# Optimization experiments

Measured on AMD Instinct MI355X. Metric: run time of the kernel, lower is better.

The kernel has to match this reference:

```python
import jax, jax.numpy as jnp
import numpy as np

# Grid / problem sizes (match init_kwargs)
B, D, H, W = 2, 64, 256, 256      # batch + spatial_shape
N = 524288                         # active voxels
IN_DIM, HID = 32, 32               # input_dim, hidden_dim
C_IN = IN_DIM + HID                # conv in-channels (64)
C_OUT = 4 * HID                    # conv out-channels (128)
OFFSETS = [(dz, dy, dx) for dz in (-1, 0, 1) for dy in (-1, 0, 1) for dx in (-1, 0, 1)]


def setup_inputs() -> dict:
    key = jax.random.key(0)
    ks = jax.random.split(key, 5)
    # Unique active-voxel coordinates: odd multiplier is a bijection mod 2^k grid size.
    total = B * D * H * W
    MULT = 2654435761  # odd => injective on arange(N) mod total (total is a power of 2)
    lin = (np.arange(N, dtype=np.int64) * MULT) % total
    b = lin // (D * H * W)
    r = lin % (D * H * W)
    z = r // (H * W)
    r = r % (H * W)
    y = r // W
    x = r % W
    coors = jnp.asarray(np.stack([b, z, y, x], axis=1).astype(np.int32))  # [N,4]
    x_features = jax.random.normal(ks[0], (N, IN_DIM), jnp.float32)
    h_features = jax.random.normal(ks[1], (N, HID), jnp.float32)
    c_features = jax.random.normal(ks[2], (N, HID), jnp.float32)
    weight = jax.random.normal(ks[3], (27, C_IN, C_OUT), jnp.float32) * 0.05
    bias = jax.random.normal(ks[4], (C_OUT,), jnp.float32) * 0.05
    return {"x_features": x_features, "h_features": h_features,
            "c_features": c_features, "weight": weight, "bias": bias,
            "coors": coors, "batch_size": B}


def _subm_conv3d(feats, weight, bias, coors):
    """Submanifold sparse 3x3x3 conv: output only at active sites;
    gather-GEMM-scatter via a dense coordinate->point-id map (the rulebook)."""
    b, z, y, x = coors[:, 0], coors[:, 1], coors[:, 2], coors[:, 3]
    pid = jnp.arange(N, dtype=jnp.int32)
    idx_map = jnp.full((B, D, H, W), -1, jnp.int32).at[b, z, y, x].set(pid)
    out = jnp.zeros((N, C_OUT), feats.dtype) + bias  # [N, 4*HID]
    for k, (dz, dy, dx) in enumerate(OFFSETS):
        nz, ny, nx = z + dz, y + dy, x + dx
        inb = (nz >= 0) & (nz < D) & (ny >= 0) & (ny < H) & (nx >= 0) & (nx < W)
        nid = idx_map[b, jnp.clip(nz, 0, D - 1), jnp.clip(ny, 0, H - 1), jnp.clip(nx, 0, W - 1)]
        nid = jnp.where(inb, nid, -1)
        valid = nid >= 0
        gathered = jnp.where(valid[:, None], feats[jnp.maximum(nid, 0)], 0.0)  # [N, C_IN]
        out = out + gathered @ weight[k]
    return out


def reference(x_features, h_features, c_features, weight, bias, coors, batch_size):
    combined = jnp.concatenate([x_features, h_features], axis=1)  # [N, C_IN]
    cc = _subm_conv3d(combined, weight, bias, coors)              # [N, 4*HID]
    cc_i, cc_f, cc_o, cc_g = jnp.split(cc, 4, axis=1)
    i = jax.nn.sigmoid(cc_i)
    f = jax.nn.sigmoid(cc_f)
    o = jax.nn.sigmoid(cc_o)
    g = jnp.tanh(cc_g)
    c_next = f * c_features + i * g
    h_next = o * jnp.tanh(c_next)
    return (h_next, c_next)
```

## Files before the change

### kernel.cpp

```cpp
#include <hip/hip_runtime.h>
#include <stdint.h>

#define N_PTS 524288
#define DQ 64
#define HQ 256
#define WQ 256
#define MAP_BYTES (2*DQ*HQ*WQ*4)
#define FEAT_BLOCKS ((N_PTS*8)/256)
#define WT_BLOCKS   ((27*64*128 + 255)/256)

typedef short bf8  __attribute__((ext_vector_type(8)));
typedef float f16v __attribute__((ext_vector_type(16)));

static __device__ __forceinline__ short f2bf(float f) {
    union { float f; uint32_t u; } v; v.f = f;
    return (short)((v.u + 0x7fffu + ((v.u >> 16) & 1u)) >> 16);
}
static __device__ __forceinline__ float fast_sigmoid(float x) {
    return 1.f / (1.f + __expf(-x));
}
static __device__ __forceinline__ float fast_tanh(float x) {
    return 1.f - 2.f / (__expf(2.f * x) + 1.f);
}

__global__ void k_prep(const float* __restrict__ xf, const float* __restrict__ hf,
                       const int* __restrict__ coors, const float* __restrict__ w,
                       short* __restrict__ fb, int* __restrict__ map,
                       short* __restrict__ wt, short* __restrict__ zp) {
    int b = blockIdx.x;
    if (b < FEAT_BLOCKS) {
        int t = b * 256 + threadIdx.x;
        int n = t >> 3, seg = t & 7;
        const float* src = (seg < 4) ? (xf + n*32 + seg*8) : (hf + n*32 + seg*8 - 32);
        float4 a = ((const float4*)src)[0];
        float4 bb = ((const float4*)src)[1];
        bf8 rv;
        rv[0]=f2bf(a.x); rv[1]=f2bf(a.y); rv[2]=f2bf(a.z); rv[3]=f2bf(a.w);
        rv[4]=f2bf(bb.x); rv[5]=f2bf(bb.y); rv[6]=f2bf(bb.z); rv[7]=f2bf(bb.w);
        ((bf8*)fb)[t] = rv;
        if (seg == 0) {
            int4 c = ((const int4*)coors)[n];
            map[((c.x*DQ + c.y)*HQ + c.z)*WQ + c.w] = n;
        }
    } else {
        int t = (b - FEAT_BLOCKS) * 256 + threadIdx.x;
        if (t < 27*64*128) {
            int jj = t & 7, c = (t >> 3) & 127, jg = (t >> 10) & 7, k = t >> 13;
            int j = jg*8 + jj;
            wt[t] = f2bf(w[(k*64 + j)*128 + c]);
        }
        if (b == FEAT_BLOCKS + WT_BLOCKS - 1 && threadIdx.x < 32)
            ((int4*)zp)[threadIdx.x] = int4{0,0,0,0};
    }
}

__launch_bounds__(256, 2)
__global__ void k_main(const int* __restrict__ map, const short* __restrict__ fb,
                       const short* __restrict__ wt, const float* __restrict__ bias,
                       const float* __restrict__ cfeat, const int* __restrict__ coors,
                       const short* __restrict__ zp, float* __restrict__ out)
{
    __shared__ short Wlds[2][8192];

    const int tid  = threadIdx.x;
    const int lane = tid & 63;
    const int wv   = tid >> 6;
    const int l31  = lane & 31;
    const int lhi  = lane >> 5;

    const int pbase = blockIdx.x * 256;
    const int p     = pbase + wv*64 + lane;

    const int4 cr = ((const int4*)coors)[p];
    const int mb0 = cr.x*DQ;

    auto probe = [&](int ko) -> int {
        int dz = ko/9 - 1, dy = (ko/3)%3 - 1, dxo = ko%3 - 1;
        int nz = cr.y + dz, ny = cr.z + dy, nx = cr.w + dxo;
        bool inb = ((unsigned)nz < (unsigned)DQ) & ((unsigned)ny < (unsigned)HQ) &
                   ((unsigned)nx < (unsigned)WQ);
        int cz = min(max(nz, 0), DQ-1);
        int cy = min(max(ny, 0), HQ-1);
        int cx = min(max(nx, 0), WQ-1);
        int nid = map[((mb0 + cz)*HQ + cy)*WQ + cx];
        return inb ? nid : -1;
    };

    auto stageW = [&](int ko) {
        const short* src = wt + ko*8192;
        #pragma unroll
        for (int i = 0; i < 4; i++) {
            int cb = i*256 + wv*64;
            __builtin_amdgcn_global_load_lds(
                (const __attribute__((address_space(1))) void*)(src + (size_t)(cb + lane)*8),
                (__attribute__((address_space(3))) void*)&Wlds[ko & 1][cb*8],
                16, 0, 0);
        }
    };

    auto gather = [&](int n0, int n1, bf8* dst) {
        const short* s0 = (n0 >= 0) ? (fb + (size_t)n0*64 + lhi*8) : (zp + lhi*8);
        const short* s1 = (n1 >= 0) ? (fb + (size_t)n1*64 + lhi*8) : (zp + lhi*8);
        #pragma unroll
        for (int j = 0; j < 4; j++) {
            dst[j]     = *(const bf8*)(s0 + j*16);
            dst[4 + j] = *(const bf8*)(s1 + j*16);
        }
    };

    f16v acc[2][4];
    #pragma unroll
    for (int mt = 0; mt < 2; mt++)
        #pragma unroll
        for (int ct = 0; ct < 4; ct++) {
            float bv = bias[ct*32 + l31];
            #pragma unroll
            for (int r = 0; r < 16; r++) acc[mt][ct][r] = bv;
        }

    stageW(0);
    int pA = probe(0);
    int pB = probe(1);
    int pr_old = probe(2);

    bf8 fA[8], fB[8];
    {
        int g0 = __shfl(pA, l31, 64);
        int g1 = __shfl(pA, l31 + 32, 64);
        gather(g0, g1, fA);
    }
    int g0n = __shfl(pB, l31, 64);
    int g1n = __shfl(pB, l31 + 32, 64);

    __builtin_amdgcn_sched_barrier(0);
    asm volatile("s_waitcnt vmcnt(0)" ::: "memory");
    __builtin_amdgcn_s_barrier();
    __builtin_amdgcn_sched_barrier(0);

#define ITER_BODY(KO, FA, FB)                                                     \
    {                                                                             \
        const int _ko = (KO);                                                     \
        if (_ko < 26) {                                                           \
            stageW(_ko + 1);                        \
            __builtin_amdgcn_sched_barrier(0);                                    \
            gather(g0n, g1n, FB);                 \
            __builtin_amdgcn_sched_barrier(0);                                    \
        }                                                                         \
        int pr_new = (_ko < 24) ? probe(_ko + 3) : -1;                \
        const int buf = _ko & 1;                                                  \
        _Pragma("unroll")                                                         \
        for (int ks = 0; ks < 4; ks++) {                                          \
            int jg = ks*2 + lhi;                                                  \
            const short* wb = &Wlds[buf][(jg*128 + l31)*8];                       \
            _Pragma("unroll")                                                     \
            for (int ct = 0; ct < 4; ct++) {                                      \
                bf8 b = *(const bf8*)(wb + ct*32*8);                              \
                acc[0][ct] = __builtin_amdgcn_mfma_f32_32x32x16_bf16(FA[ks],     b, acc[0][ct], 0, 0, 0); \
                acc[1][ct] = __builtin_amdgcn_mfma_f32_32x32x16_bf16(FA[4 + ks], b, acc[1][ct], 0, 0, 0); \
            }                                                                     \
        }                                                                         \
        if (_ko < 25) {                                 \
            g0n = __shfl(pr_old, l31, 64);                                        \
            g1n = __shfl(pr_old, l31 + 32, 64);                                   \
            pr_old = pr_new;                                                      \
        }                                                                         \
        if (_ko < 26) {                                                           \
            __builtin_amdgcn_sched_barrier(0);                                    \
            \
            if (_ko < 24) { asm volatile("s_waitcnt vmcnt(9)" ::: "memory"); }    \
            else          { asm volatile("s_waitcnt vmcnt(8)" ::: "memory"); }    \
            __builtin_amdgcn_s_barrier();                                         \
            __builtin_amdgcn_sched_barrier(0);                                    \
        }                                                                         \
    }

    #pragma unroll 1
    for (int ko = 0; ko < 26; ko += 2) {
        ITER_BODY(ko,     fA, fB)
        ITER_BODY(ko + 1, fB, fA)
    }
    ITER_BODY(26, fA, fB)
#undef ITER_BODY

    #pragma unroll
    for (int mt = 0; mt < 2; mt++) {
        #pragma unroll
        for (int r = 0; r < 16; r++) {
            int row = (r & 3) + 8*(r >> 2) + 4*lhi;
            int pp  = pbase + wv*64 + mt*32 + row;
            float gi = acc[mt][0][r];
            float gf = acc[mt][1][r];
            float go = acc[mt][2][r];
            float gg = acc[mt][3][r];
            float cv = cfeat[pp*32 + l31];
            float si = fast_sigmoid(gi);
            float sf = fast_sigmoid(gf);
            float so = fast_sigmoid(go);
            float tg = fast_tanh(gg);
            float cn = sf*cv + si*tg;
            float hn = so * fast_tanh(cn);
            out[pp*32 + l31] = hn;
            out[N_PTS*32 + pp*32 + l31] = cn;
        }
    }
}

extern "C" void kernel_launch(void* const* d_in, const int* in_sizes, int n_in,
                              void* d_out, int out_size, void* d_ws, size_t ws_size,
                              hipStream_t stream) {
    const float* xf    = (const float*)d_in[0];
    const float* hf    = (const float*)d_in[1];
    const float* cf    = (const float*)d_in[2];
    const float* w     = (const float*)d_in[3];
    const float* bias  = (const float*)d_in[4];
    const int*   coors = (const int*)d_in[5];
    float* out = (float*)d_out;

    char* base = (char*)d_ws;
    int*   map    = (int*)base;
    short* fb     = (short*)(base + MAP_BYTES);
    short* wtb    = (short*)(base + 100663296);
    short* zp     = (short*)(base + 101105664);

    hipMemsetAsync(map, 0xFF, MAP_BYTES, stream);
    k_prep<<<FEAT_BLOCKS + WT_BLOCKS, 256, 0, stream>>>(xf, hf, coors, w, fb, map, wtb, zp);
    k_main<<<N_PTS/256, 256, 0, stream>>>(map, fb, wtb, bias, cf, coors, zp, out);
}
```

Baseline: 524.1 us.

## Pad coordinate map with halo, shift ids by one, triple-buffer weight staging

```diff
diff --git a/kernel.cpp b/kernel.cpp
--- a/kernel.cpp
+++ b/kernel.cpp
@@ -5,12 +5,22 @@
 #define DQ 64
 #define HQ 256
 #define WQ 256
-#define MAP_BYTES (2*DQ*HQ*WQ*4)
+#define MD 66
+#define MH 258
+#define MW 258
+#define MAP_INTS (2*MD*MH*MW)
+#define MAP_PAD  35145856
 #define FEAT_BLOCKS ((N_PTS*8)/256)
 #define WT_BLOCKS   ((27*64*128 + 255)/256)
 
 typedef short bf8  __attribute__((ext_vector_type(8)));
 typedef float f16v __attribute__((ext_vector_type(16)));
+
+static __device__ const int DOFF[27] = {
+    -66823, -66822, -66821, -66565, -66564, -66563, -66307, -66306, -66305,
+      -259,   -258,   -257,     -1,      0,      1,    257,    258,    259,
+     66305,  66306,  66307,  66563,  66564,  66565,  66821,  66822,  66823
+};
 
 static __device__ __forceinline__ short f2bf(float f) {
     union { float f; uint32_t u; } v; v.f = f;
@@ -26,7 +36,7 @@
 __global__ void k_prep(const float* __restrict__ xf, const float* __restrict__ hf,
                        const int* __restrict__ coors, const float* __restrict__ w,
                        short* __restrict__ fb, int* __restrict__ map,
-                       short* __restrict__ wt, short* __restrict__ zp) {
+                       short* __restrict__ wt) {
     int b = blockIdx.x;
     if (b < FEAT_BLOCKS) {
         int t = b * 256 + threadIdx.x;
@@ -37,10 +47,11 @@
         bf8 rv;
         rv[0]=f2bf(a.x); rv[1]=f2bf(a.y); rv[2]=f2bf(a.z); rv[3]=f2bf(a.w);
         rv[4]=f2bf(bb.x); rv[5]=f2bf(bb.y); rv[6]=f2bf(bb.z); rv[7]=f2bf(bb.w);
-        ((bf8*)fb)[t] = rv;
+        ((bf8*)fb)[(n+1)*8 + seg] = rv;
         if (seg == 0) {
             int4 c = ((const int4*)coors)[n];
-            map[((c.x*DQ + c.y)*HQ + c.z)*WQ + c.w] = n;
+            int mb = ((c.x*MD + c.y+1)*MH + c.z+1)*MW + (c.w+1);
+            map[mb] = n + 1;
         }
     } else {
         int t = (b - FEAT_BLOCKS) * 256 + threadIdx.x;
@@ -49,8 +60,6 @@
             int j = jg*8 + jj;
             wt[t] = f2bf(w[(k*64 + j)*128 + c]);
         }
-        if (b == FEAT_BLOCKS + WT_BLOCKS - 1 && threadIdx.x < 32)
-            ((int4*)zp)[threadIdx.x] = int4{0,0,0,0};
     }
 }
 
@@ -58,9 +67,9 @@
 __global__ void k_main(const int* __restrict__ map, const short* __restrict__ fb,
                        const short* __restrict__ wt, const float* __restrict__ bias,
                        const float* __restrict__ cfeat, const int* __restrict__ coors,
-                       const short* __restrict__ zp, float* __restrict__ out)
+                       float* __restrict__ out)
 {
-    __shared__ short Wlds[2][8192];
+    __shared__ short Wlds[3][8192];
 
     const int tid  = threadIdx.x;
     const int lane = tid & 63;
@@ -72,35 +81,26 @@
     const int p     = pbase + wv*64 + lane;
 
     const int4 cr = ((const int4*)coors)[p];
-    const int mb0 = cr.x*DQ;
-
-    auto probe = [&](int ko) -> int {
-        int dz = ko/9 - 1, dy = (ko/3)%3 - 1, dxo = ko%3 - 1;
-        int nz = cr.y + dz, ny = cr.z + dy, nx = cr.w + dxo;
-        bool inb = ((unsigned)nz < (unsigned)DQ) & ((unsigned)ny < (unsigned)HQ) &
-                   ((unsigned)nx < (unsigned)WQ);
-        int cz = min(max(nz, 0), DQ-1);
-        int cy = min(max(ny, 0), HQ-1);
-        int cx = min(max(nx, 0), WQ-1);
-        int nid = map[((mb0 + cz)*HQ + cy)*WQ + cx];
-        return inb ? nid : -1;
-    };
+    const int mb = ((cr.x*MD + cr.y+1)*MH + cr.z+1)*MW + (cr.w+1);
+
+    auto probe = [&](int ko) -> int { return map[mb + DOFF[ko]]; };
 
     auto stageW = [&](int ko) {
         const short* src = wt + ko*8192;
+        short* dst = &Wlds[ko % 3][0];
         #pragma unroll
         for (int i = 0; i < 4; i++) {
             int cb = i*256 + wv*64;
             __builtin_amdgcn_global_load_lds(
                 (const __attribute__((address_space(1))) void*)(src + (size_t)(cb + lane)*8),
-                (__attribute__((address_space(3))) void*)&Wlds[ko & 1][cb*8],
+                (__attribute__((address_space(3))) void*)(dst + (size_t)cb*8),
                 16, 0, 0);
         }
     };
 
-    auto gather = [&](int n0, int n1, bf8* dst) {
-        const short* s0 = (n0 >= 0) ? (fb + (size_t)n0*64 + lhi*8) : (zp + lhi*8);
-        const short* s1 = (n1 >= 0) ? (fb + (size_t)n1*64 + lhi*8) : (zp + lhi*8);
+    auto gather = [&](int v0, int v1, bf8* dst) {
+        const short* s0 = fb + (size_t)v0*64 + lhi*8;
+        const short* s1 = fb + (size_t)v1*64 + lhi*8;
         #pragma unroll
         for (int j = 0; j < 4; j++) {
             dst[j]     = *(const bf8*)(s0 + j*16);
@@ -119,39 +119,34 @@
         }
 
     stageW(0);
+    stageW(1);
+    __builtin_amdgcn_sched_barrier(0);
     int pA = probe(0);
     int pB = probe(1);
     int pr_old = probe(2);
 
     bf8 fA[8], fB[8];
-    {
-        int g0 = __shfl(pA, l31, 64);
-        int g1 = __shfl(pA, l31 + 32, 64);
-        gather(g0, g1, fA);
-    }
+    gather(__shfl(pA, l31, 64), __shfl(pA, l31 + 32, 64), fA);
     int g0n = __shfl(pB, l31, 64);
     int g1n = __shfl(pB, l31 + 32, 64);
 
     __builtin_amdgcn_sched_barrier(0);
-    asm volatile("s_waitcnt vmcnt(0)" ::: "memory");
+    asm volatile("s_waitcnt vmcnt(11)" ::: "memory");
     __builtin_amdgcn_s_barrier();
     __builtin_amdgcn_sched_barrier(0);
 
 #define ITER_BODY(KO, FA, FB)                                                     \
     {                                                                             \
         const int _ko = (KO);                                                     \
-        if (_ko < 26) {                                                           \
-            stageW(_ko + 1);                        \
-            __builtin_amdgcn_sched_barrier(0);                                    \
-            gather(g0n, g1n, FB);                 \
-            __builtin_amdgcn_sched_barrier(0);                                    \
-        }                                                                         \
-        int pr_new = (_ko < 24) ? probe(_ko + 3) : -1;                \
-        const int buf = _ko & 1;                                                  \
+        if (_ko < 25) stageW(_ko + 2);          \
+        __builtin_amdgcn_sched_barrier(0);                                        \
+        if (_ko < 26) gather(g0n, g1n, FB);       \
+        int pr_new = (_ko < 24) ? probe(_ko + 3) : 0;                 \
+        const short* wbuf = &Wlds[_ko % 3][0];                                    \
         _Pragma("unroll")                                                         \
         for (int ks = 0; ks < 4; ks++) {                                          \
             int jg = ks*2 + lhi;                                                  \
-            const short* wb = &Wlds[buf][(jg*128 + l31)*8];                       \
+            const short* wb = wbuf + (jg*128 + l31)*8;                            \
             _Pragma("unroll")                                                     \
             for (int ct = 0; ct < 4; ct++) {                                      \
                 bf8 b = *(const bf8*)(wb + ct*32*8);                              \
@@ -159,7 +154,7 @@
                 acc[1][ct] = __builtin_amdgcn_mfma_f32_32x32x16_bf16(FA[4 + ks], b, acc[1][ct], 0, 0, 0); \
             }                                                                     \
         }                                                                         \
-        if (_ko < 25) {                                 \
+        if (_ko < 25) {                                  \
             g0n = __shfl(pr_old, l31, 64);                                        \
             g1n = __shfl(pr_old, l31 + 32, 64);                                   \
             pr_old = pr_new;                                                      \
@@ -167,8 +162,9 @@
         if (_ko < 26) {                                                           \
             __builtin_amdgcn_sched_barrier(0);                                    \
             \
-            if (_ko < 24) { asm volatile("s_waitcnt vmcnt(9)" ::: "memory"); }    \
-            else          { asm volatile("s_waitcnt vmcnt(8)" ::: "memory"); }    \
+            if (_ko < 24)       { asm volatile("s_waitcnt vmcnt(22)" ::: "memory"); } \
+            else if (_ko == 24) { asm volatile("s_waitcnt vmcnt(21)" ::: "memory"); } \
+            else                { asm volatile("s_waitcnt vmcnt(16)" ::: "memory"); } \
             __builtin_amdgcn_s_barrier();                                         \
             __builtin_amdgcn_sched_barrier(0);                                    \
         }                                                                         \
@@ -218,11 +214,10 @@
 
     char* base = (char*)d_ws;
     int*   map    = (int*)base;
-    short* fb     = (short*)(base + MAP_BYTES);
-    short* wtb    = (short*)(base + 100663296);
-    short* zp     = (short*)(base + 101105664);
-
-    hipMemsetAsync(map, 0xFF, MAP_BYTES, stream);
-    k_prep<<<FEAT_BLOCKS + WT_BLOCKS, 256, 0, stream>>>(xf, hf, coors, w, fb, map, wtb, zp);
-    k_main<<<N_PTS/256, 256, 0, stream>>>(map, fb, wtb, bias, cf, coors, zp, out);
-}
+    short* fb     = (short*)(base + MAP_PAD);
+    short* wtb    = (short*)(base + MAP_PAD + (size_t)(N_PTS+1)*128);
+
+    hipMemsetAsync(base, 0, MAP_PAD + 128, stream);
+    k_prep<<<FEAT_BLOCKS + WT_BLOCKS, 256, 0, stream>>>(xf, hf, coors, w, fb, map, wtb);
+    k_main<<<N_PTS/256, 256, 0, stream>>>(map, fb, wtb, bias, cf, coors, out);
+}
```

Result: no change. 522.0 us (-0.4%).
